# Kernel optimization log

Hardware: AMD Instinct MI355X
Metric: run time of the kernel (lower is better)

The kernel has to match this reference:

```python
import jax, jax.numpy as jnp
import numpy as np

B, C, H, W, NCH = 2, 256, 48, 48, 12


def setup_inputs() -> dict:
    key = jax.random.key(0)
    k1, k2, k3, k4, k5 = jax.random.split(key, 5)
    gray_feature = jax.random.normal(k1, (B, C, H, W), jnp.float32)
    rgb_feature = jax.random.normal(k2, (B, C, H, W), jnp.float32)
    rgb_image = jax.random.uniform(k3, (B, 3, H, W), jnp.float32)
    # one-hot segmentation labels: random class id per pixel in [0, NCH)
    gcls = jax.random.randint(k4, (B, H, W), 0, NCH)
    rcls = jax.random.randint(k5, (B, H, W), 0, NCH)
    gray_label = jax.nn.one_hot(gcls, NCH, axis=1, dtype=jnp.float32)
    rgb_label = jax.nn.one_hot(rcls, NCH, axis=1, dtype=jnp.float32)
    return dict(gray_feature=gray_feature, rgb_feature=rgb_feature,
                rgb_image=rgb_image, gray_label=gray_label, rgb_label=rgb_label)


def _masked_normalize(feat, maskf):
    # feat: [b,c,N], maskf: [b,N] in {0,1}. Subtract per-channel masked mean,
    # then divide each masked pixel's feature vector by its channel-norm.
    cnt = maskf.sum(-1)                                            # [b]
    mean = jnp.einsum('bcn,bn->bc', feat, maskf) / jnp.maximum(cnt, 1.0)[:, None]
    bar = (feat - mean[:, :, None]) * maskf[:, None, :]            # zero outside mask
    norm = jnp.sqrt(jnp.sum(bar * bar, axis=1))                    # [b,N]
    unit = bar / jnp.where(norm > 0, norm, 1.0)[:, None, :]
    return unit, cnt


def reference(gray_feature, rgb_feature, rgb_image, gray_label, rgb_label):
    b, c, h, w = gray_feature.shape
    N = h * w
    gf = gray_feature.reshape(b, c, N)
    rf = rgb_feature.reshape(b, c, N)
    img = rgb_image.reshape(b, 3, N)
    gms = gray_label.reshape(b, -1, N) > 0.5   # [b,NCH,N] bool
    rms = rgb_label.reshape(b, -1, N) > 0.5
    canvas = -jnp.ones((b, 3, N), gray_feature.dtype)
    NEG = jnp.asarray(-1e30, gray_feature.dtype)
    for k in range(1, 12):  # classes 1..11, matching the torch loop
        gm = gms[:, k]                                     # [b,N]
        rm = rms[:, k]
        gmf = gm.astype(gf.dtype)
        rmf = rm.astype(rf.dtype)
        gn, cg = _masked_normalize(gf, gmf)                # [b,c,N]
        rn, cr = _masked_normalize(rf, rmf)
        # normalized correlation between gray and rgb masked pixels
        corr = jnp.einsum('bci,bcj->bij', gn, rn)          # [b,N,N]
        logits = jnp.where(rm[:, None, :], corr, NEG)      # softmax over rgb-mask pixels
        sm = jax.nn.softmax(logits, axis=-1)
        out = jnp.einsum('bij,bcj->bci', sm, img)          # [b,3,N]
        # skip condition from torch: needs >=2 pixels on each side
        valid = (cg > 1) & (cr > 1)                        # [b]
        write = gm & valid[:, None]                        # [b,N]
        canvas = jnp.where(write[:, None, :], out, canvas)
    return canvas.reshape(b, 3, h, w)
```

## Files before the change

### kernel.cpp

```cpp
#include <hip/hip_runtime.h>
#include <math.h>

#define BN 2
#define CC 256
#define NN 2304
#define KK 12
#define MC 320
#define KT 32
#define QT 32
#define TNQ (MC / QT)

#define OFF_CNT_G   0
#define OFF_CNT_R   32
#define OFF_IDX_G   64
#define OFF_CPS_G   (OFF_IDX_G + BN * KK * MC)
#define OFF_CPS_R   (OFF_CPS_G + BN * NN)
#define OFF_MSUM_G  (OFF_CPS_R + BN * NN)
#define OFF_MSUM_R  (OFF_MSUM_G + BN * KK * CC)
#define OFF_IMGC    (OFF_MSUM_R + BN * KK * CC)
#define OFF_INV_G   (OFF_IMGC + BN * KK * 3 * MC)
#define OFF_INV_R   (OFF_INV_G + BN * KK * MC)
#define OFF_UCG     (OFF_INV_R + BN * KK * MC)
#define OFF_UCR     (OFF_UCG + BN * KK * MC * CC)

__global__ __launch_bounds__(256) void prep_mean_kernel(
        const float* __restrict__ gf, const float* __restrict__ rf,
        const float* __restrict__ img, const float* __restrict__ gl,
        const float* __restrict__ rl, float* __restrict__ out,
        int* cnt_g, int* cnt_r, int* idx_g, int* cps_g, int* cps_r,
        float* imgc, float* msum_g, float* msum_r) {
    __shared__ int wcnt[4];
    __shared__ float wsum[4][KK];
    int bid = blockIdx.x, tid = threadIdx.x;
    int lane = tid & 63, wid = tid >> 6;

    if (bid < 48) {
        int type = bid / (BN * KK);
        int rem = bid % (BN * KK);
        int b = rem / KK, k = rem % KK;
        const float* lp = (type ? rl : gl) + ((size_t)(b * KK + k)) * NN;
        int* cps = type ? cps_r : cps_g;
        int* cnt = type ? cnt_r : cnt_g;
        int base = 0;
        for (int c0 = 0; c0 < NN; c0 += 256) {
            int i = c0 + tid;
            bool p = lp[i] > 0.5f;
            unsigned long long m = __ballot(p);
            int rank = __popcll(m & ((1ull << lane) - 1));
            if (lane == 0) wcnt[wid] = __popcll(m);
            __syncthreads();
            int pre = 0;
            for (int w = 0; w < wid; ++w) pre += wcnt[w];
            int tot = wcnt[0] + wcnt[1] + wcnt[2] + wcnt[3];
            if (p) {
                int pos = base + pre + rank;
                cps[b * NN + i] = (k << 16) | pos;
                if (pos < MC) {
                    if (type) {
                        for (int ch = 0; ch < 3; ++ch)
                            imgc[((b * KK + k) * 3 + ch) * MC + pos] =
                                img[((size_t)(b * 3 + ch)) * NN + i];
                    } else {
                        idx_g[(b * KK + k) * MC + pos] = i;
                    }
                }
            }
            base += tot;
            __syncthreads();
        }
        if (tid == 0) cnt[b * KK + k] = base;
    } else {
        int u = bid - 48;
        if (u < 54) out[u * 256 + tid] = -1.0f;
        int type = u >> 9;
        int rem = u & 511;
        int b = rem >> 8, c = rem & 255;
        const float* f = (type ? rf : gf) + ((size_t)(b * CC + c)) * NN;
        const float* lab = (type ? rl : gl) + ((size_t)b) * KK * NN;
        float* msum = type ? msum_r : msum_g;

        float acc[KK];
        #pragma unroll
        for (int kk = 0; kk < KK; ++kk) acc[kk] = 0.f;
        for (int i = tid; i < NN; i += 256) {
            float v = f[i];
            #pragma unroll
            for (int kk = 0; kk < KK; ++kk) acc[kk] += lab[(size_t)kk * NN + i] * v;
        }
        #pragma unroll
        for (int kk = 0; kk < KK; ++kk) {
            #pragma unroll
            for (int o = 32; o; o >>= 1) acc[kk] += __shfl_xor(acc[kk], o, 64);
        }
        if (lane == 0) {
            #pragma unroll
            for (int kk = 0; kk < KK; ++kk) wsum[wid][kk] = acc[kk];
        }
        __syncthreads();
        if (tid < KK)
            msum[(b * KK + tid) * CC + c] =
                wsum[0][tid] + wsum[1][tid] + wsum[2][tid] + wsum[3][tid];
    }
}

__global__ __launch_bounds__(256) void center_kernel(
        const float* __restrict__ gf, const float* __restrict__ rf,
        const int* __restrict__ cps_g, const int* __restrict__ cps_r,
        const int* __restrict__ cnt_g, const int* __restrict__ cnt_r,
        const float* __restrict__ msum_g, const float* __restrict__ msum_r,
        float* ucg, float* ucr, float* inv_g, float* inv_r) {
    const int PCH = NN / 32;
    int blk = blockIdx.x;
    int type = blk / (BN * PCH);
    int rem = blk % (BN * PCH);
    int b = rem / PCH, chunk = rem % PCH;
    int i0 = chunk * 32;
    const float* f = type ? rf : gf;
    const int* cps = type ? cps_r : cps_g;
    const int* cnt = type ? cnt_r : cnt_g;
    const float* msum = type ? msum_r : msum_g;
    float* uc = type ? ucr : ucg;
    float* invc = type ? inv_r : inv_g;

    __shared__ float lmean[KK * 257];
    __shared__ float tile[64 * 33];

    int tid = threadIdx.x;
    for (int x = tid; x < KK * CC; x += 256) {
        int k = x >> 8, c = x & 255;
        float cn = fmaxf((float)cnt[b * KK + k], 1.f);
        lmean[k * 257 + c] = msum[(b * KK + k) * CC + c] / cn;
    }
    int p = tid >> 3, q = tid & 7;
    int pl = tid & 31, cb = tid >> 5;
    int kcpos = cps[b * NN + i0 + p];
    int kc = kcpos >> 16, pos = kcpos & 0xFFFF;
    bool wr = pos < MC;
    float ss = 0.f;
    float* ub = uc + ((size_t)((b * KK + kc) * MC + (wr ? pos : MC - 1))) * CC;
    for (int cc = 0; cc < 4; ++cc) {
        __syncthreads();
        for (int j = 0; j < 8; ++j) {
            int c = cb * 8 + j;
            tile[c * 33 + pl] = f[((size_t)(b * CC + cc * 64 + c)) * NN + i0 + pl];
        }
        __syncthreads();
        #pragma unroll
        for (int h = 0; h < 2; ++h) {
            int c0 = q * 8 + h * 4;
            float4 v;
            v.x = tile[(c0 + 0) * 33 + p] - lmean[kc * 257 + cc * 64 + c0 + 0];
            v.y = tile[(c0 + 1) * 33 + p] - lmean[kc * 257 + cc * 64 + c0 + 1];
            v.z = tile[(c0 + 2) * 33 + p] - lmean[kc * 257 + cc * 64 + c0 + 2];
            v.w = tile[(c0 + 3) * 33 + p] - lmean[kc * 257 + cc * 64 + c0 + 3];
            ss += v.x * v.x + v.y * v.y + v.z * v.z + v.w * v.w;
            if (wr) *(float4*)&ub[cc * 64 + c0] = v;
        }
    }
    ss += __shfl_xor(ss, 1, 64);
    ss += __shfl_xor(ss, 2, 64);
    ss += __shfl_xor(ss, 4, 64);
    if (q == 0 && wr)
        invc[(b * KK + kc) * MC + pos] = (ss > 0.f) ? rsqrtf(ss) : 1.0f;
}

__global__ __launch_bounds__(256) void corr_out_kernel(
        const int* __restrict__ cnt_g, const int* __restrict__ cnt_r,
        const int* __restrict__ idx_g,
        const float* __restrict__ ucg, const float* __restrict__ ucr,
        const float* __restrict__ inv_g, const float* __restrict__ inv_r,
        const float* __restrict__ imgc, float* __restrict__ out) {
    int tq = blockIdx.x % TNQ;
    int k = (blockIdx.x / TNQ) % KK;
    int b = blockIdx.x / (TNQ * KK);
    if (k == 0) return;
    int bk = b * KK + k;
    int cg_ = cnt_g[bk], cr_ = cnt_r[bk];
    if (cg_ <= 1 || cr_ <= 1) return;
    int Mg = min(cg_, MC), Mr = min(cr_, MC);
    int q0 = tq * QT;
    if (q0 >= Mg) return;

    __shared__ float Af[CC * 34];
    __shared__ float Bs[KT * 68];

    int tid = threadIdx.x;
    {
        int r = tid >> 3, c8 = tid & 7;
        const float* rowA = ucg + ((size_t)(bk * MC + q0 + r)) * CC;
        #pragma unroll
        for (int j = 0; j < 8; ++j) {
            int c0 = j * 32 + c8 * 4;
            float4 va = *(const float4*)&rowA[c0];
            Af[(c0 + 0) * 34 + r] = va.x;
            Af[(c0 + 1) * 34 + r] = va.y;
            Af[(c0 + 2) * 34 + r] = va.z;
            Af[(c0 + 3) * 34 + r] = va.w;
        }
    }
    int tx = tid & 15, ty = tid >> 4;
    float invi[2];
    #pragma unroll
    for (int x = 0; x < 2; ++x) invi[x] = inv_g[bk * MC + q0 + ty * 2 + x];
    const float* im0 = imgc + (bk * 3 + 0) * MC;
    const float* im1 = imgc + (bk * 3 + 1) * MC;
    const float* im2 = imgc + (bk * 3 + 2) * MC;

    float s[2] = {0.f, 0.f}, p0[2] = {0.f, 0.f}, p1[2] = {0.f, 0.f}, p2[2] = {0.f, 0.f};
    int r2 = tid >> 2, c4 = tid & 3;

    for (int k0 = 0; k0 < Mr; k0 += 64) {
        float acc[2][4];
        #pragma unroll
        for (int x = 0; x < 2; ++x)
            #pragma unroll
            for (int y = 0; y < 4; ++y) acc[x][y] = 0.f;

        for (int kcc = 0; kcc < CC; kcc += KT) {
            __syncthreads();
            const float* rowB = ucr + ((size_t)(bk * MC + k0 + r2)) * CC + kcc;
            #pragma unroll
            for (int jj = 0; jj < 2; ++jj) {
                int ch = jj * 16 + c4 * 4;
                float4 vb = *(const float4*)&rowB[ch];
                Bs[(ch + 0) * 68 + r2] = vb.x;
                Bs[(ch + 1) * 68 + r2] = vb.y;
                Bs[(ch + 2) * 68 + r2] = vb.z;
                Bs[(ch + 3) * 68 + r2] = vb.w;
            }
            __syncthreads();
            #pragma unroll 8
            for (int kk = 0; kk < KT; ++kk) {
                float2 av = *(const float2*)&Af[(kcc + kk) * 34 + ty * 2];
                float4 bv = *(const float4*)&Bs[kk * 68 + tx * 4];
                acc[0][0] += av.x * bv.x; acc[0][1] += av.x * bv.y;
                acc[0][2] += av.x * bv.z; acc[0][3] += av.x * bv.w;
                acc[1][0] += av.y * bv.x; acc[1][1] += av.y * bv.y;
                acc[1][2] += av.y * bv.z; acc[1][3] += av.y * bv.w;
            }
        }
        float4 w0 = *(const float4*)&im0[k0 + tx * 4];
        float4 w1 = *(const float4*)&im1[k0 + tx * 4];
        float4 w2 = *(const float4*)&im2[k0 + tx * 4];
        float4 vj = *(const float4*)&inv_r[bk * MC + k0 + tx * 4];
        float wj0[4] = {w0.x, w0.y, w0.z, w0.w};
        float wj1[4] = {w1.x, w1.y, w1.z, w1.w};
        float wj2[4] = {w2.x, w2.y, w2.z, w2.w};
        float vjj[4] = {vj.x, vj.y, vj.z, vj.w};
        #pragma unroll
        for (int x = 0; x < 2; ++x) {
            #pragma unroll
            for (int y = 0; y < 4; ++y) {
                int col = k0 + tx * 4 + y;
                float e = (col < Mr) ? __expf(acc[x][y] * invi[x] * vjj[y]) : 0.f;
                s[x] += e;
                p0[x] += e * wj0[y];
                p1[x] += e * wj1[y];
                p2[x] += e * wj2[y];
            }
        }
    }
    #pragma unroll
    for (int o = 1; o <= 8; o <<= 1) {
        #pragma unroll
        for (int x = 0; x < 2; ++x) {
            s[x]  += __shfl_xor(s[x],  o, 64);
            p0[x] += __shfl_xor(p0[x], o, 64);
            p1[x] += __shfl_xor(p1[x], o, 64);
            p2[x] += __shfl_xor(p2[x], o, 64);
        }
    }
    if (tx == 0) {
        #pragma unroll
        for (int x = 0; x < 2; ++x) {
            int row = q0 + ty * 2 + x;
            if (row < Mg) {
                int gi = idx_g[bk * MC + row];
                float inv = 1.0f / s[x];
                out[((size_t)(b * 3 + 0)) * NN + gi] = p0[x] * inv;
                out[((size_t)(b * 3 + 1)) * NN + gi] = p1[x] * inv;
                out[((size_t)(b * 3 + 2)) * NN + gi] = p2[x] * inv;
            }
        }
    }
}

extern "C" void kernel_launch(void* const* d_in, const int* in_sizes, int n_in,
                              void* d_out, int out_size, void* d_ws, size_t ws_size,
                              hipStream_t stream) {
    const float* gf  = (const float*)d_in[0];
    const float* rf  = (const float*)d_in[1];
    const float* img = (const float*)d_in[2];
    const float* gl  = (const float*)d_in[3];
    const float* rl  = (const float*)d_in[4];
    float* out = (float*)d_out;
    float* ws = (float*)d_ws;

    int*   cnt_g  = (int*)(ws + OFF_CNT_G);
    int*   cnt_r  = (int*)(ws + OFF_CNT_R);
    int*   idx_g  = (int*)(ws + OFF_IDX_G);
    int*   cps_g  = (int*)(ws + OFF_CPS_G);
    int*   cps_r  = (int*)(ws + OFF_CPS_R);
    float* msum_g = ws + OFF_MSUM_G;
    float* msum_r = ws + OFF_MSUM_R;
    float* imgc   = ws + OFF_IMGC;
    float* inv_g  = ws + OFF_INV_G;
    float* inv_r  = ws + OFF_INV_R;
    float* ucg    = ws + OFF_UCG;
    float* ucr    = ws + OFF_UCR;

    prep_mean_kernel<<<48 + 2 * BN * CC, 256, 0, stream>>>(
        gf, rf, img, gl, rl, out, cnt_g, cnt_r, idx_g, cps_g, cps_r,
        imgc, msum_g, msum_r);
    center_kernel<<<2 * BN * (NN / 32), 256, 0, stream>>>(
        gf, rf, cps_g, cps_r, cnt_g, cnt_r, msum_g, msum_r,
        ucg, ucr, inv_g, inv_r);
    corr_out_kernel<<<BN * KK * TNQ, 256, 0, stream>>>(
        cnt_g, cnt_r, idx_g, ucg, ucr, inv_g, inv_r, imgc, out);
}
```

Measured before the change: 123.4 us.

## Retile correlation kernel to 8 query rows per block for more blocks

The correlation/softmax kernel now gives each block 8 gray rows instead of 32, with one row per 32-lane group and 128 rgb columns per tile. This gives four times as many blocks, to fill the GPU for a small per-class problem. The staging layout is also reorganised, and index clamping replaces padded reads. To make the clamped and padded reads safe, the prep kernel now zero-fills the unused tail of the compacted index, image and inverse-norm buffers. Each block reuses its B tile across fewer rows, so global and LDS traffic for the rgb features rises.

Result: faster. 117.1 us (-5.2%).

```diff
diff --git a/kernel.cpp b/kernel.cpp
--- a/kernel.cpp
+++ b/kernel.cpp
@@ -6,9 +6,9 @@
 #define NN 2304
 #define KK 12
 #define MC 320
-#define KT 32
-#define QT 32
-#define TNQ (MC / QT)
+#define QT 8
+#define KTL 128
+#define KCH 32
 
 #define OFF_CNT_G   0
 #define OFF_CNT_R   32
@@ -28,7 +28,8 @@
         const float* __restrict__ img, const float* __restrict__ gl,
         const float* __restrict__ rl, float* __restrict__ out,
         int* cnt_g, int* cnt_r, int* idx_g, int* cps_g, int* cps_r,
-        float* imgc, float* msum_g, float* msum_r) {
+        float* imgc, float* inv_g, float* inv_r,
+        float* msum_g, float* msum_r) {
     __shared__ int wcnt[4];
     __shared__ float wsum[4][KK];
     int bid = blockIdx.x, tid = threadIdx.x;
@@ -69,6 +70,18 @@
             __syncthreads();
         }
         if (tid == 0) cnt[b * KK + k] = base;
+        int start = base < MC ? base : MC;
+        for (int pos = start + tid; pos < MC; pos += 256) {
+            if (type) {
+                for (int ch = 0; ch < 3; ++ch)
+                    imgc[((b * KK + k) * 3 + ch) * MC + pos] = 0.f;
+            } else {
+                idx_g[(b * KK + k) * MC + pos] = 0;
+            }
+        }
+        float* invc = type ? inv_r : inv_g;
+        for (int pos = tid; pos < MC; pos += 256)
+            invc[(b * KK + k) * MC + pos] = 0.f;
     } else {
         int u = bid - 48;
         if (u < 54) out[u * 256 + tid] = -1.0f;
@@ -170,6 +183,7 @@
         const float* __restrict__ ucg, const float* __restrict__ ucr,
         const float* __restrict__ inv_g, const float* __restrict__ inv_r,
         const float* __restrict__ imgc, float* __restrict__ out) {
+    const int TNQ = MC / QT;
     int tq = blockIdx.x % TNQ;
     int k = (blockIdx.x / TNQ) % KK;
     int b = blockIdx.x / (TNQ * KK);
@@ -181,106 +195,93 @@
     int q0 = tq * QT;
     if (q0 >= Mg) return;
 
-    __shared__ float Af[CC * 34];
-    __shared__ float Bs[KT * 68];
+    __shared__ float Af[QT * (CC + 4)];
+    __shared__ float Bs[KCH * (KTL + 4)];
 
     int tid = threadIdx.x;
     {
-        int r = tid >> 3, c8 = tid & 7;
-        const float* rowA = ucg + ((size_t)(bk * MC + q0 + r)) * CC;
-        #pragma unroll
-        for (int j = 0; j < 8; ++j) {
-            int c0 = j * 32 + c8 * 4;
-            float4 va = *(const float4*)&rowA[c0];
-            Af[(c0 + 0) * 34 + r] = va.x;
-            Af[(c0 + 1) * 34 + r] = va.y;
-            Af[(c0 + 2) * 34 + r] = va.z;
-            Af[(c0 + 3) * 34 + r] = va.w;
-        }
-    }
-    int tx = tid & 15, ty = tid >> 4;
-    float invi[2];
-    #pragma unroll
-    for (int x = 0; x < 2; ++x) invi[x] = inv_g[bk * MC + q0 + ty * 2 + x];
+        int r = tid >> 5, c32 = tid & 31;
+        int rowi = q0 + r; if (rowi > MC - 1) rowi = MC - 1;
+        const float* rowA = ucg + ((size_t)(bk * MC + rowi)) * CC;
+        #pragma unroll
+        for (int j = 0; j < 2; ++j) {
+            int c0 = c32 * 8 + j * 4;
+            *(float4*)&Af[r * (CC + 4) + c0] = *(const float4*)&rowA[c0];
+        }
+    }
+
+    int ty = tid >> 5;
+    int tx = tid & 31;
+    int rowg = q0 + ty; if (rowg > MC - 1) rowg = MC - 1;
+    float invi = inv_g[bk * MC + rowg];
     const float* im0 = imgc + (bk * 3 + 0) * MC;
     const float* im1 = imgc + (bk * 3 + 1) * MC;
     const float* im2 = imgc + (bk * 3 + 2) * MC;
-
-    float s[2] = {0.f, 0.f}, p0[2] = {0.f, 0.f}, p1[2] = {0.f, 0.f}, p2[2] = {0.f, 0.f};
-    int r2 = tid >> 2, c4 = tid & 3;
-
-    for (int k0 = 0; k0 < Mr; k0 += 64) {
-        float acc[2][4];
-        #pragma unroll
-        for (int x = 0; x < 2; ++x)
-            #pragma unroll
-            for (int y = 0; y < 4; ++y) acc[x][y] = 0.f;
-
-        for (int kcc = 0; kcc < CC; kcc += KT) {
+    float s = 0.f, p0 = 0.f, p1 = 0.f, p2 = 0.f;
+
+    for (int k0 = 0; k0 < Mr; k0 += KTL) {
+        float acc[4] = {0.f, 0.f, 0.f, 0.f};
+        for (int kcc = 0; kcc < CC; kcc += KCH) {
             __syncthreads();
-            const float* rowB = ucr + ((size_t)(bk * MC + k0 + r2)) * CC + kcc;
-            #pragma unroll
-            for (int jj = 0; jj < 2; ++jj) {
-                int ch = jj * 16 + c4 * 4;
-                float4 vb = *(const float4*)&rowB[ch];
-                Bs[(ch + 0) * 68 + r2] = vb.x;
-                Bs[(ch + 1) * 68 + r2] = vb.y;
-                Bs[(ch + 2) * 68 + r2] = vb.z;
-                Bs[(ch + 3) * 68 + r2] = vb.w;
+            {
+                int col = tid >> 1, half = tid & 1;
+                int colr = k0 + col; if (colr > MC - 1) colr = MC - 1;
+                const float* rowB = ucr + ((size_t)(bk * MC + colr)) * CC + kcc + half * 16;
+                #pragma unroll
+                for (int j = 0; j < 4; ++j) {
+                    float4 vb = *(const float4*)&rowB[j * 4];
+                    int c = half * 16 + j * 4;
+                    Bs[(c + 0) * (KTL + 4) + col] = vb.x;
+                    Bs[(c + 1) * (KTL + 4) + col] = vb.y;
+                    Bs[(c + 2) * (KTL + 4) + col] = vb.z;
+                    Bs[(c + 3) * (KTL + 4) + col] = vb.w;
+                }
             }
             __syncthreads();
-            #pragma unroll 8
-            for (int kk = 0; kk < KT; ++kk) {
-                float2 av = *(const float2*)&Af[(kcc + kk) * 34 + ty * 2];
-                float4 bv = *(const float4*)&Bs[kk * 68 + tx * 4];
-                acc[0][0] += av.x * bv.x; acc[0][1] += av.x * bv.y;
-                acc[0][2] += av.x * bv.z; acc[0][3] += av.x * bv.w;
-                acc[1][0] += av.y * bv.x; acc[1][1] += av.y * bv.y;
-                acc[1][2] += av.y * bv.z; acc[1][3] += av.y * bv.w;
+            #pragma unroll
+            for (int kk = 0; kk < KCH; ++kk) {
+                float av = Af[ty * (CC + 4) + kcc + kk];
+                float4 bv = *(const float4*)&Bs[kk * (KTL + 4) + tx * 4];
+                acc[0] += av * bv.x;
+                acc[1] += av * bv.y;
+                acc[2] += av * bv.z;
+                acc[3] += av * bv.w;
             }
         }
-        float4 w0 = *(const float4*)&im0[k0 + tx * 4];
-        float4 w1 = *(const float4*)&im1[k0 + tx * 4];
-        float4 w2 = *(const float4*)&im2[k0 + tx * 4];
-        float4 vj = *(const float4*)&inv_r[bk * MC + k0 + tx * 4];
+        int kidx = k0 + tx * 4; if (kidx > MC - 4) kidx = MC - 4;
+        float4 w0 = *(const float4*)&im0[kidx];
+        float4 w1 = *(const float4*)&im1[kidx];
+        float4 w2 = *(const float4*)&im2[kidx];
+        float4 vj = *(const float4*)&inv_r[bk * MC + kidx];
         float wj0[4] = {w0.x, w0.y, w0.z, w0.w};
         float wj1[4] = {w1.x, w1.y, w1.z, w1.w};
         float wj2[4] = {w2.x, w2.y, w2.z, w2.w};
         float vjj[4] = {vj.x, vj.y, vj.z, vj.w};
         #pragma unroll
-        for (int x = 0; x < 2; ++x) {
-            #pragma unroll
-            for (int y = 0; y < 4; ++y) {
-                int col = k0 + tx * 4 + y;
-                float e = (col < Mr) ? __expf(acc[x][y] * invi[x] * vjj[y]) : 0.f;
-                s[x] += e;
-                p0[x] += e * wj0[y];
-                p1[x] += e * wj1[y];
-                p2[x] += e * wj2[y];
-            }
+        for (int y = 0; y < 4; ++y) {
+            int col = k0 + tx * 4 + y;
+            float e = (col < Mr) ? __expf(acc[y] * invi * vjj[y]) : 0.f;
+            s += e;
+            p0 += e * wj0[y];
+            p1 += e * wj1[y];
+            p2 += e * wj2[y];
         }
     }
     #pragma unroll
-    for (int o = 1; o <= 8; o <<= 1) {
-        #pragma unroll
-        for (int x = 0; x < 2; ++x) {
-            s[x]  += __shfl_xor(s[x],  o, 64);
-            p0[x] += __shfl_xor(p0[x], o, 64);
-            p1[x] += __shfl_xor(p1[x], o, 64);
-            p2[x] += __shfl_xor(p2[x], o, 64);
-        }
+    for (int o = 1; o <= 16; o <<= 1) {
+        s  += __shfl_xor(s,  o, 64);
+        p0 += __shfl_xor(p0, o, 64);
+        p1 += __shfl_xor(p1, o, 64);
+        p2 += __shfl_xor(p2, o, 64);
     }
     if (tx == 0) {
-        #pragma unroll
-        for (int x = 0; x < 2; ++x) {
-            int row = q0 + ty * 2 + x;
-            if (row < Mg) {
-                int gi = idx_g[bk * MC + row];
-                float inv = 1.0f / s[x];
-                out[((size_t)(b * 3 + 0)) * NN + gi] = p0[x] * inv;
-                out[((size_t)(b * 3 + 1)) * NN + gi] = p1[x] * inv;
-                out[((size_t)(b * 3 + 2)) * NN + gi] = p2[x] * inv;
-            }
+        int row = q0 + ty;
+        if (row < Mg) {
+            int gi = idx_g[bk * MC + row];
+            float inv = 1.0f / s;
+            out[((size_t)(b * 3 + 0)) * NN + gi] = p0 * inv;
+            out[((size_t)(b * 3 + 1)) * NN + gi] = p1 * inv;
+            out[((size_t)(b * 3 + 2)) * NN + gi] = p2 * inv;
         }
     }
 }
@@ -311,10 +312,10 @@
 
     prep_mean_kernel<<<48 + 2 * BN * CC, 256, 0, stream>>>(
         gf, rf, img, gl, rl, out, cnt_g, cnt_r, idx_g, cps_g, cps_r,
-        imgc, msum_g, msum_r);
+        imgc, inv_g, inv_r, msum_g, msum_r);
     center_kernel<<<2 * BN * (NN / 32), 256, 0, stream>>>(
         gf, rf, cps_g, cps_r, cnt_g, cnt_r, msum_g, msum_r,
         ucg, ucr, inv_g, inv_r);
-    corr_out_kernel<<<BN * KK * TNQ, 256, 0, stream>>>(
+    corr_out_kernel<<<BN * KK * (MC / QT), 256, 0, stream>>>(
         cnt_g, cnt_r, idx_g, ucg, ucr, inv_g, inv_r, imgc, out);
 }
```
